# Performance work log

Hardware: AMD Instinct MI355X
Metric: run time of the kernel (lower is better)

The kernel has to match this reference:

```python
import jax, jax.numpy as jnp
import numpy as np

B, T, H, N_HEADS, HEAD_D = 16, 512, 1024, 16, 64
N_SKILLS, N_ITEMS = 50, 1000
VOCAB = 4 + 2 * N_ITEMS  # 2004
LN_EPS = 1e-3            # keras LayerNormalization default
PAD_NEG = -float(2 ** 32)


def position_encoding(length, hidden):
    # official transformer get_position_encoding: [sin | cos], then interleaved
    half = hidden // 2
    pos = jnp.arange(length, dtype=jnp.float32)[:, None]
    log_inc = np.log(1e4) / (half - 1)
    inv_ts = jnp.exp(jnp.arange(half, dtype=jnp.float32) * -log_inc)
    ang = pos * inv_ts[None, :]  # [T, H/2]
    pe = jnp.zeros((length, hidden), dtype=jnp.float32)
    pe = pe.at[:, 0::2].set(jnp.sin(ang))
    pe = pe.at[:, 1::2].set(jnp.cos(ang))
    return pe


def setup_inputs() -> dict:
    key = jax.random.key(0)
    ks = jax.random.split(key, 12)
    rng = np.random.default_rng(0)
    # binary Q-matrix [skills, items]; ensure every item has >=1 skill
    Qb = (rng.random((N_SKILLS, N_ITEMS)) < 0.1).astype(np.float32)
    Qb[rng.integers(0, N_SKILLS, size=N_ITEMS), np.arange(N_ITEMS)] = 1.0
    s = 0.02
    return {
        'prob_x': jax.random.randint(ks[0], (B, T), 4, VOCAB, dtype=jnp.int32),
        'prob_y2': jax.random.randint(ks[1], (B, T), 4, VOCAB, dtype=jnp.int32),
        'emb': jax.random.normal(ks[2], (VOCAB, H), jnp.float32) * s,
        'wq': jax.random.normal(ks[3], (H, N_HEADS, HEAD_D), jnp.float32) * s,
        'wk': jax.random.normal(ks[4], (H, N_HEADS, HEAD_D), jnp.float32) * s,
        'wv': jax.random.normal(ks[5], (H, N_HEADS, HEAD_D), jnp.float32) * s,
        'wo': jax.random.normal(ks[6], (N_HEADS, HEAD_D, H), jnp.float32) * s,
        'ln_gamma': jnp.ones((H,), jnp.float32),
        'ln_beta': jnp.zeros((H,), jnp.float32),
        'w_hid': jax.random.normal(ks[7], (H, 2 * N_SKILLS), jnp.float32) * s,
        'b_hid': jnp.zeros((2 * N_SKILLS,), jnp.float32),
        'w_skill': jax.random.normal(ks[8], (2 * N_SKILLS, N_SKILLS), jnp.float32) * s,
        'b_skill': jnp.zeros((N_SKILLS,), jnp.float32),
        'w_prob': jax.random.normal(ks[9], (N_SKILLS, N_ITEMS), jnp.float32) * s,
        'b_prob': jnp.zeros((N_ITEMS,), jnp.float32),
        'q_matrix': jnp.asarray(Qb),
    }


def reference(prob_x, prob_y2, emb, wq, wk, wv, wo, ln_gamma, ln_beta,
              w_hid, b_hid, w_skill, b_skill, w_prob, b_prob, q_matrix):
    Bq, Tq = prob_x.shape
    pid = (prob_x - 4) // 2        # item ids [B,T]
    next_pid = (prob_y2 - 4) // 2  # [B,T]

    x = emb[prob_x] + position_encoding(Tq, emb.shape[1])  # [B,T,H]

    # QKV projections (DenseEinsum, no bias)
    q = jnp.einsum('bth,hnd->btnd', x, wq) * (HEAD_D ** -0.5)
    k = jnp.einsum('bth,hnd->btnd', x, wk)
    v = jnp.einsum('bth,hnd->btnd', x, wv)

    logits = jnp.einsum('btnd,bfnd->bnft', k, q)  # [B,N,F,T]

    # causal future mask: 0 on/below diag, -inf above (1 - exp(1/tri - 1))
    causal = jnp.where(jnp.tril(jnp.ones((Tq, Tq), bool)), 0.0, -jnp.inf)
    logits = logits + causal[None, None]

    # item-item common-skill mask: -inf where items share no skill, 0 otherwise
    qtq = q_matrix.T @ q_matrix  # [I,I]
    items_items = jnp.where(qtq > 0, 0.0, -jnp.inf)
    sub = items_items[pid[:, 1:, None], pid[:, None, 1:]]  # [B,T-1,T-1]
    csm = jnp.pad(sub, ((0, 0), (1, 0), (1, 0)), constant_values=PAD_NEG)
    logits = logits + csm[:, None]  # broadcast over heads

    weights = jax.nn.softmax(logits, axis=-1)  # [B,N,F,T]
    attn = jnp.einsum('bnft,btnd->bfnd', weights, v)
    attn = jnp.einsum('bfnd,ndh->bfh', attn, wo)

    # add & layer-norm (keras default eps=1e-3)
    y = x + attn
    mu = jnp.mean(y, axis=-1, keepdims=True)
    var = jnp.var(y, axis=-1, keepdims=True)
    y = (y - mu) * jax.lax.rsqrt(var + LN_EPS) * ln_gamma + ln_beta

    h = jax.nn.relu(y @ w_hid + b_hid)
    skills = h @ w_skill + b_skill
    problems = jax.nn.sigmoid(skills @ w_prob + b_prob)  # [B,T,I]
    # einsum('abi,abi->ab', problems, one_hot(next_pid)) == gather
    out = jnp.take_along_axis(problems, next_pid[..., None], axis=-1)[..., 0]
    return out
```

## Files before the change

kernel.cpp:

```cpp
#include <hip/hip_runtime.h>
#include <hip/hip_bf16.h>

#define Bb 16
#define Tt 512
#define Hh 1024
#define NHd 16
#define HD 64
#define BT (Bb*Tt)
#define NSK 50
#define NIT 1000

typedef __attribute__((ext_vector_type(8))) short bf16x8;
typedef __attribute__((ext_vector_type(4))) float f32x4;
typedef unsigned short u16;
typedef unsigned int u32;
typedef unsigned long long u64;

__device__ inline u16 f2bf(float x){
  union { float f; u32 u; } v; v.f = x;
  u32 r = v.u + 0x7fffu + ((v.u >> 16) & 1u);
  return (u16)(r >> 16);
}
__device__ inline float bf2f(u32 u){
  union { u32 uu; float f; } v; v.uu = u << 16; return v.f;
}
__device__ inline u32 pack2bf(float lo, float hi){
  return (u32)f2bf(lo) | ((u32)f2bf(hi) << 16);
}
__device__ inline void gload_lds16(const void* g, void* l){
  __builtin_amdgcn_global_load_lds(
    (const __attribute__((address_space(1))) u32*)g,
    (__attribute__((address_space(3))) u32*)l, 16, 0, 0);
}

__global__ __launch_bounds__(256) void k_wT_all(
    const float* __restrict__ wq, const float* __restrict__ wk,
    const float* __restrict__ wv, const float* __restrict__ wo,
    const float* __restrict__ wh, const float* __restrict__ gamma,
    const float* __restrict__ beta,
    const int* __restrict__ prob_x, const float* __restrict__ qm,
    const float* __restrict__ wp,
    u16* __restrict__ wqkvT, u16* __restrict__ woT, u16* __restrict__ whT,
    float2* __restrict__ uvp, u64* __restrict__ pmask, float* __restrict__ wpt){
  int z = blockIdx.z;
  int tid = threadIdx.x;
  if (z == 5){
    if (blockIdx.y) return;
    int i = blockIdx.x*256 + tid;
    int pid = (prob_x[i] - 4) >> 1;
    u64 m = 0ull;
    #pragma unroll
    for (int s = 0; s < NSK; s++)
      if (qm[s*NIT + pid] != 0.f) m |= (1ull << s);
    pmask[i] = m;
    return;
  }
  if (z == 6){
    int blk = blockIdx.y*32 + blockIdx.x;
    if (blk >= 250) return;
    int p = blk*4 + (tid >> 6), lane = tid & 63;
    if (lane < NSK) wpt[(size_t)p*64 + lane] = wp[(size_t)lane*NIT + p];
    return;
  }
  const float* src; u16* dst; int C = 1024; float scale = 1.f; bool useg = false;
  if      (z == 0){ src = wq; dst = wqkvT;                       scale = 0.125f; }
  else if (z == 1){ src = wk; dst = wqkvT + (size_t)1024*1024; }
  else if (z == 2){ src = wv; dst = wqkvT + (size_t)2*1024*1024; }
  else if (z == 3){ src = wo; dst = woT; }
  else            { src = wh; dst = whT; C = 100; useg = true; if (blockIdx.x >= 4) return; }

  __shared__ float tile[32][33];
  int tx = tid & 31, ty = tid >> 5;
  int c0 = blockIdx.x*32, r0 = blockIdx.y*32;
  #pragma unroll
  for (int i = 0; i < 32; i += 8){
    int r = r0 + ty + i, cc = c0 + tx;
    tile[ty+i][tx] = (cc < C) ? src[(size_t)r*C + cc] : 0.f;
  }
  __syncthreads();
  float gmul = useg ? gamma[r0 + tx] : scale;
  #pragma unroll
  for (int i = 0; i < 32; i += 8){
    int cc = c0 + ty + i, rr = r0 + tx;
    dst[(size_t)cc*1024 + rr] = f2bf(tile[tx][ty+i] * gmul);
  }
  if (useg && tid < 32){
    int j = tid;
    float us = 0.f, vs = 0.f;
    #pragma unroll
    for (int k = 0; k < 32; k++){
      float wv2 = tile[k][j];
      us += gamma[r0 + k] * wv2;
      vs += beta[r0 + k] * wv2;
    }
    uvp[(size_t)blockIdx.y*128 + c0 + j] = make_float2(us, vs);
  }
}

__global__ __launch_bounds__(256) void k_build_x2(
    const int* __restrict__ prob_x, const float* __restrict__ emb,
    u16* __restrict__ xb){
  int bt = blockIdx.x, tid = threadIdx.x;
  int t = bt & (Tt-1);
  int ix = prob_x[bt];
  int h = tid*4;
  float4 e = *(const float4*)(emb + (size_t)ix*Hh + h);
  const float LOG_INC = 0.0180241495f;
  int j0 = h >> 1;
  float a0 = (float)t * __expf(-(float)j0 * LOG_INC);
  float a1 = (float)t * __expf(-(float)(j0+1) * LOG_INC);
  alignas(8) u16 tmp[4] = { f2bf(e.x + __sinf(a0)), f2bf(e.y + __cosf(a0)),
                            f2bf(e.z + __sinf(a1)), f2bf(e.w + __cosf(a1)) };
  *(uint2*)(xb + (size_t)bt*Hh + h) = *(const uint2*)tmp;
}

#define MFMA_(d, va, vb) d = __builtin_amdgcn_mfma_f32_16x16x32_bf16(va, vb, d, 0, 0, 0)

__device__ __forceinline__ void gemm128x256_core(
    const u16* __restrict__ A, const u16* __restrict__ Bt,
    int row0, int col0, char* lds, f32x4 (&acc)[4][4])
{
  const int tid = threadIdx.x, w = tid >> 6, lane = tid & 63;
  const int c = lane & 15, g = lane >> 4;
  const int wm = w >> 2, wn = w & 3;
  const int srl = lane >> 3, scb = lane & 7;
  const int kbsw = scb ^ srl;

  #define STAGE6(buf, k0)                                                        \
    do {                                                                         \
      char* _da = lds + (buf)*49152 + w*2048;                                    \
      char* _db = lds + (buf)*49152 + 16384 + w*4096;                            \
      _Pragma("unroll")                                                          \
      for (int i = 0; i < 2; i++)                                                \
        gload_lds16(A + (size_t)(row0 + 16*w + 8*i + srl)*1024 + (k0) + kbsw*8,  \
                    _da + i*1024);                                               \
      _Pragma("unroll")                                                          \
      for (int i = 0; i < 4; i++)                                                \
        gload_lds16(Bt + (size_t)(col0 + 32*w + 8*i + srl)*1024 + (k0) + kbsw*8, \
                    _db + i*1024);                                               \
    } while (0)

  STAGE6(0, 0);
  STAGE6(1, 64);
  asm volatile("s_waitcnt vmcnt(6)" ::: "memory");
  __builtin_amdgcn_s_barrier();

  #pragma unroll
  for (int kt = 0; kt < 16; ++kt){
    const int buf = kt % 3;
    if (kt + 2 < 16) STAGE6((kt + 2) % 3, (kt + 2)*64);

    bf16x8 af[2][4], bf[2][4];
    #pragma unroll
    for (int kh = 0; kh < 2; kh++){
      #pragma unroll
      for (int mi = 0; mi < 4; mi++){
        int r = 64*wm + 16*mi + c;
        af[kh][mi] = *(const bf16x8*)(lds + buf*49152 + r*128 + (((kh*4 + g) ^ (c & 7))*16));
      }
      #pragma unroll
      for (int ni = 0; ni < 4; ni++){
        int r = 64*wn + 16*ni + c;
        bf[kh][ni] = *(const bf16x8*)(lds + buf*49152 + 16384 + r*128 + (((kh*4 + g) ^ (c & 7))*16));
      }
    }
    __builtin_amdgcn_s_setprio(1);
    #pragma unroll
    for (int kh = 0; kh < 2; kh++)
      #pragma unroll
      for (int mi = 0; mi < 4; mi++)
        #pragma unroll
        for (int ni = 0; ni < 4; ni++) MFMA_(acc[mi][ni], af[kh][mi], bf[kh][ni]);
    __builtin_amdgcn_s_setprio(0);

    if (kt < 15){
      if (kt < 14) asm volatile("s_waitcnt vmcnt(6)" ::: "memory");
      else         asm volatile("s_waitcnt vmcnt(0)" ::: "memory");
      __builtin_amdgcn_s_barrier();
    }
  }
  #undef STAGE6
}

__global__ __launch_bounds__(512) void k_gemm_qkv3(
    const u16* __restrict__ A, const u16* __restrict__ Bt,
    u16* __restrict__ qb, u16* __restrict__ kb, u16* __restrict__ vtb)
{
  extern __shared__ char lds[];
  int lin = blockIdx.x;
  int xcd = lin & 7, j = lin >> 3;
  int by = xcd*8 + (j & 7);
  int bx = j >> 3;
  const int row0 = by*128, col0 = bx*256;

  f32x4 acc[4][4];
  #pragma unroll
  for (int mi = 0; mi < 4; mi++)
    #pragma unroll
    for (int ni = 0; ni < 4; ni++) acc[mi][ni] = (f32x4){0.f,0.f,0.f,0.f};

  gemm128x256_core(A, Bt, row0, col0, lds, acc);

  const int tid = threadIdx.x, w = tid >> 6, lane = tid & 63;
  const int c = lane & 15, g = lane >> 4;
  const int wm = w >> 2, wn = w & 3;
  int seg = col0 >> 10;
  int colL0 = col0 & 1023;
  if (seg < 2){
    u16* C = seg ? kb : qb;
    #pragma unroll
    for (int mi = 0; mi < 4; mi++){
      int m0 = row0 + 64*wm + 16*mi + 4*g;
      int bb = m0 >> 9, t0 = m0 & (Tt-1);
      #pragma unroll
      for (int ni = 0; ni < 4; ni++){
        int col = colL0 + 64*wn + 16*ni + c;
        int hd_ = col >> 6, d_ = col & 63;
        u16* base = C + (((size_t)bb*NHd + hd_)*Tt + t0)*HD + d_;
        #pragma unroll
        for (int r = 0; r < 4; r++) base[(size_t)r*HD] = f2bf(acc[mi][ni][r]);
      }
    }
  } else {
    #pragma unroll
    for (int mi = 0; mi < 4; mi++){
      int m0 = row0 + 64*wm + 16*mi + 4*g;
      int bb = m0 >> 9, t0 = m0 & (Tt-1);
      #pragma unroll
      for (int ni = 0; ni < 4; ni++){
        int col = colL0 + 64*wn + 16*ni + c;
        int hd_ = col >> 6, d_ = col & 63;
        alignas(8) u16 tmp[4];
        #pragma unroll
        for (int r = 0; r < 4; r++) tmp[r] = f2bf(acc[mi][ni][r]);
        *(uint2*)(vtb + (((size_t)bb*NHd + hd_)*HD + d_)*Tt + t0) = *(const uint2*)tmp;
      }
    }
  }
}

__global__ __launch_bounds__(512) void k_gemm_wo3(
    const u16* __restrict__ A, const u16* __restrict__ Bt,
    u16* __restrict__ C, const u16* __restrict__ res, float2* __restrict__ stats)
{
  extern __shared__ char lds[];
  int lin = blockIdx.x;
  int xcd = lin & 7, j = lin >> 3;
  int by = xcd*8 + (j & 7);
  int bx = j >> 3;
  const int row0 = by*128, col0 = bx*256;

  f32x4 acc[4][4];
  #pragma unroll
  for (int mi = 0; mi < 4; mi++)
    #pragma unroll
    for (int ni = 0; ni < 4; ni++) acc[mi][ni] = (f32x4){0.f,0.f,0.f,0.f};

  gemm128x256_core(A, Bt, row0, col0, lds, acc);

  const int tid = threadIdx.x, w = tid >> 6, lane = tid & 63;
  const int c = lane & 15, g = lane >> 4;
  const int wm = w >> 2, wn = w & 3;

  float s1[4][4], s2[4][4];
  #pragma unroll
  for (int mi = 0; mi < 4; mi++)
    #pragma unroll
    for (int r = 0; r < 4; r++){ s1[mi][r] = 0.f; s2[mi][r] = 0.f; }

  #pragma unroll
  for (int mi = 0; mi < 4; mi++){
    int m0 = row0 + 64*wm + 16*mi + 4*g;
    #pragma unroll
    for (int ni = 0; ni < 4; ni++){
      int col = col0 + 64*wn + 16*ni + c;
      #pragma unroll
      for (int r = 0; r < 4; r++){
        size_t idx = (size_t)(m0 + r)*Hh + col;
        float yv = acc[mi][ni][r] + bf2f((u32)res[idx]);
        C[idx] = f2bf(yv);
        s1[mi][r] += yv; s2[mi][r] += yv*yv;
      }
    }
  }
  #pragma unroll
  for (int mi = 0; mi < 4; mi++)
    #pragma unroll
    for (int r = 0; r < 4; r++){
      #pragma unroll
      for (int off = 1; off < 16; off <<= 1){
        s1[mi][r] += __shfl_xor(s1[mi][r], off);
        s2[mi][r] += __shfl_xor(s2[mi][r], off);
      }
    }
  __syncthreads();
  float (*sStat)[4][2] = (float(*)[4][2])lds;
  if (c == 0){
    #pragma unroll
    for (int mi = 0; mi < 4; mi++)
      #pragma unroll
      for (int r = 0; r < 4; r++){
        int ml = 64*wm + 16*mi + 4*g + r;
        sStat[ml][wn][0] = s1[mi][r];
        sStat[ml][wn][1] = s2[mi][r];
      }
  }
  __syncthreads();
  if (tid < 128){
    float a = sStat[tid][0][0] + sStat[tid][1][0] + sStat[tid][2][0] + sStat[tid][3][0];
    float b = sStat[tid][0][1] + sStat[tid][1][1] + sStat[tid][2][1] + sStat[tid][3][1];
    stats[(size_t)(row0 + tid)*4 + bx] = make_float2(a, b);
  }
}

__global__ __launch_bounds__(256) void k_gemm_hidden(
    const u16* __restrict__ A, const u16* __restrict__ Bt,
    const float2* __restrict__ stats, const float2* __restrict__ uvp,
    const float* __restrict__ b_hid, u16* __restrict__ C)
{
  __shared__ u16 sA[32*64];
  __shared__ u16 sB[128*64];
  __shared__ float sMu[32][2];
  __shared__ float2 sUV[128];
  const int tid = threadIdx.x, w = tid >> 6, lane = tid & 63;
  const int c = lane & 15, g = lane >> 4;
  const int row0 = blockIdx.x*32;
  const int srl = lane >> 3, scb = lane & 7;

  if (tid < 32){
    float m = 0.f, q = 0.f;
    #pragma unroll
    for (int cb = 0; cb < 4; cb++){
      float2 s = stats[(size_t)(row0 + tid)*4 + cb];
      m += s.x; q += s.y;
    }
    float mu = m * (1.f/Hh);
    float var = q * (1.f/Hh) - mu*mu;
    sMu[tid][0] = mu;
    sMu[tid][1] = rsqrtf(var + 1e-3f);
  }
  if (tid < 128){
    float us = 0.f, vs = 0.f;
    #pragma unroll 8
    for (int cb = 0; cb < 32; cb++){
      float2 p = uvp[(size_t)cb*128 + tid];
      us += p.x; vs += p.y;
    }
    float2 r = make_float2(0.f, 0.f);
    if (tid < 100){ r.x = us; r.y = vs + b_hid[tid]; }
    sUV[tid] = r;
  }

  f32x4 acc[2][2];
  #pragma unroll
  for (int mi = 0; mi < 2; mi++)
    #pragma unroll
    for (int ni = 0; ni < 2; ni++) acc[mi][ni] = (f32x4){0.f,0.f,0.f,0.f};

  for (int k0 = 0; k0 < 1024; k0 += 64){
    __syncthreads();
    {
      int arow = 8*w + srl;
      int kblk = scb ^ (arow & 7);
      gload_lds16(A + (size_t)(row0 + arow)*1024 + k0 + kblk*8,
                  (char*)sA + w*1024);
      #pragma unroll
      for (int i = 0; i < 4; i++){
        int brow = 32*w + 8*i + srl;
        int kb2 = scb ^ (brow & 7);
        gload_lds16(Bt + (size_t)brow*1024 + k0 + kb2*8,
                    (char*)sB + w*4096 + i*1024);
      }
    }
    __syncthreads();

    #pragma unroll
    for (int kh = 0; kh < 2; kh++){
      bf16x8 af[2], bf[2];
      #pragma unroll
      for (int mi = 0; mi < 2; mi++){
        int r = 16*mi + c;
        af[mi] = *(const bf16x8*)((char*)sA + r*128 + (((4*kh + g) ^ (r & 7))*16));
      }
      #pragma unroll
      for (int ni = 0; ni < 2; ni++){
        int r = 32*w + 16*ni + c;
        bf[ni] = *(const bf16x8*)((char*)sB + r*128 + (((4*kh + g) ^ (r & 7))*16));
      }
      #pragma unroll
      for (int mi = 0; mi < 2; mi++)
        #pragma unroll
        for (int ni = 0; ni < 2; ni++)
          acc[mi][ni] = __builtin_amdgcn_mfma_f32_16x16x32_bf16(af[mi], bf[ni], acc[mi][ni], 0, 0, 0);
    }
  }

  #pragma unroll
  for (int mi = 0; mi < 2; mi++){
    #pragma unroll
    for (int ni = 0; ni < 2; ni++){
      int col = 32*w + 16*ni + c;
      float2 uvv = sUV[col];
      #pragma unroll
      for (int r = 0; r < 4; r++){
        int ml = 16*mi + 4*g + r;
        float mu = sMu[ml][0], inv = sMu[ml][1];
        float h = fmaxf(inv*(acc[mi][ni][r] - mu*uvv.x) + uvv.y, 0.f);
        C[(size_t)(row0 + ml)*128 + col] = f2bf(h);
      }
    }
  }
}

__global__ __launch_bounds__(256, 3) void k_flash(
    const u16* __restrict__ qb, const u16* __restrict__ kb,
    const u16* __restrict__ vtb, const u64* __restrict__ pmask,
    u16* __restrict__ o)
{
  __shared__ u16 sK[2][64*64];
  __shared__ u16 sV[2][64*64];
  __shared__ u16 sP[4][32*64];

  const int tid = threadIdx.x;
  const int w = tid >> 6, lane = tid & 63;
  const int c = lane & 15, g = lane >> 4;
  const int bn = blockIdx.x;
  const int Fblk = 3 - blockIdx.y;
  const int b = bn >> 4, n = bn & 15;
  const int f0w = Fblk*128 + w*32;

  bf16x8 qf[2][2];
  #pragma unroll
  for (int fb = 0; fb < 2; fb++){
    const u16* qrow = qb + ((size_t)bn*Tt + f0w + 16*fb + c)*HD + 8*g;
    qf[fb][0] = *(const bf16x8*)(qrow);
    qf[fb][1] = *(const bf16x8*)(qrow + 32);
  }

  const u64* pmb = pmask + b*Tt;
  int frow[2]; u64 mf[2];
  #pragma unroll
  for (int fb = 0; fb < 2; fb++){ frow[fb] = f0w + 16*fb + c; mf[fb] = pmb[frow[fb]]; }

  f32x4 O[2][4];
  #pragma unroll
  for (int fb = 0; fb < 2; fb++)
    #pragma unroll
    for (int dt = 0; dt < 4; dt++) O[fb][dt] = (f32x4){0.f,0.f,0.f,0.f};
  float m_run[2] = {-1e30f, -1e30f};
  float l_run[2] = {0.f, 0.f};

  const char* kbase = (const char*)(kb + (size_t)bn*Tt*HD);
  const char* vbase = (const char*)(vtb + (size_t)bn*HD*Tt);
  char* sPw = (char*)(sP[w]);

  const int srow0 = 16*w + (lane >> 3);
  const int scb = lane & 7;

  #define STAGE(buf, T0)                                                          \
    {                                                                             \
      _Pragma("unroll")                                                           \
      for (int i = 0; i < 2; i++){                                                \
        int row = srow0 + 8*i;                                                    \
        int cb = scb ^ (row & 7);                                                 \
        gload_lds16(kbase + (size_t)((T0) + row)*128 + cb*16,                     \
                    (char*)sK[buf] + w*2048 + i*1024);                            \
        gload_lds16(vbase + (size_t)row*1024 + (T0)*2 + cb*16,                    \
                    (char*)sV[buf] + w*2048 + i*1024);                            \
      }                                                                           \
    }

  const int nT = 2*Fblk + 2;
  STAGE(0, 0)
  __syncthreads();
  int cur = 0;

  for (int it = 0; it < nT; ++it){
    const int t0 = it * 64;
    if (it + 1 < nT) STAGE(cur^1, (it+1)*64)

    if (t0 <= f0w + 31){
      const char* sKc = (const char*)sK[cur];
      const char* sVc = (const char*)sV[cur];

      f32x4 S[2][4];
      __builtin_amdgcn_s_setprio(1);
      #pragma unroll
      for (int ts = 0; ts < 4; ts++){
        int tl = ts*16 + c;
        const char* kr = sKc + tl*128;
        int sw = (tl & 7) << 4;
        bf16x8 kf0 = *(const bf16x8*)(kr + ((g*16) ^ sw));
        bf16x8 kf1 = *(const bf16x8*)(kr + ((64 + g*16) ^ sw));
        #pragma unroll
        for (int fb = 0; fb < 2; fb++){
          f32x4 a = (f32x4){0.f,0.f,0.f,0.f};
          a = __builtin_amdgcn_mfma_f32_16x16x32_bf16(kf0, qf[fb][0], a, 0, 0, 0);
          a = __builtin_amdgcn_mfma_f32_16x16x32_bf16(kf1, qf[fb][1], a, 0, 0, 0);
          S[fb][ts] = a;
        }
      }
      __builtin_amdgcn_s_setprio(0);

      u64 pmt[4][4];
      #pragma unroll
      for (int ts = 0; ts < 4; ts++){
        const u64* pp = pmb + t0 + 16*ts + 4*g;
        pmt[ts][0] = pp[0]; pmt[ts][1] = pp[1];
        pmt[ts][2] = pp[2]; pmt[ts][3] = pp[3];
      }

      #pragma unroll
      for (int fb = 0; fb < 2; fb++){
        int f = frow[fb];
        u64 mfr = mf[fb];
        #pragma unroll
        for (int ts = 0; ts < 4; ts++){
          #pragma unroll
          for (int r = 0; r < 4; r++){
            int t = t0 + 16*ts + 4*g + r;
            bool ok = (f == 0) ? (t == 0)
                     : (t > 0 && t <= f && ((pmt[ts][r] & mfr) != 0ull));
            if (!ok) S[fb][ts][r] = -1e30f;
          }
        }
        float mx = -1e30f;
        #pragma unroll
        for (int ts = 0; ts < 4; ts++)
          #pragma unroll
          for (int r = 0; r < 4; r++) mx = fmaxf(mx, S[fb][ts][r]);
        mx = fmaxf(mx, __shfl_xor(mx, 16));
        mx = fmaxf(mx, __shfl_xor(mx, 32));
        float mnew = fmaxf(m_run[fb], mx);
        float al = __expf(m_run[fb] - mnew);
        m_run[fb] = mnew;
        l_run[fb] *= al;
        #pragma unroll
        for (int dt = 0; dt < 4; dt++) O[fb][dt] *= al;

        int prow = 16*fb + c;
        int swz = (prow & 7) << 4;
        float lsum = 0.f;
        #pragma unroll
        for (int ts = 0; ts < 4; ts++){
          float p0 = __expf(S[fb][ts][0] - mnew);
          float p1 = __expf(S[fb][ts][1] - mnew);
          float p2 = __expf(S[fb][ts][2] - mnew);
          float p3 = __expf(S[fb][ts][3] - mnew);
          lsum += (p0 + p1) + (p2 + p3);
          uint2 dw = { pack2bf(p0, p1), pack2bf(p2, p3) };
          *(uint2*)(sPw + prow*128 + ((32*ts + 8*g) ^ swz)) = dw;
        }
        l_run[fb] += lsum;
      }

      bf16x8 pa[2][2];
      #pragma unroll
      for (int fb = 0; fb < 2; fb++){
        int prow = 16*fb + c;
        int swz = (prow & 7) << 4;
        const char* pr = sPw + prow*128;
        pa[fb][0] = *(const bf16x8*)(pr + ((16*g) ^ swz));
        pa[fb][1] = *(const bf16x8*)(pr + ((64 + 16*g) ^ swz));
      }
      __builtin_amdgcn_s_setprio(1);
      #pragma unroll
      for (int dt = 0; dt < 4; dt++){
        int vl = dt*16 + c;
        const char* vr = sVc + vl*128;
        int swv = (vl & 7) << 4;
        bf16x8 vf0 = *(const bf16x8*)(vr + ((g*16) ^ swv));
        bf16x8 vf1 = *(const bf16x8*)(vr + ((64 + g*16) ^ swv));
        #pragma unroll
        for (int fb = 0; fb < 2; fb++){
          O[fb][dt] = __builtin_amdgcn_mfma_f32_16x16x32_bf16(vf0, pa[fb][0], O[fb][dt], 0, 0, 0);
          O[fb][dt] = __builtin_amdgcn_mfma_f32_16x16x32_bf16(vf1, pa[fb][1], O[fb][dt], 0, 0, 0);
        }
      }
      __builtin_amdgcn_s_setprio(0);
    }

    __syncthreads();
    cur ^= 1;
  }
  #undef STAGE

  #pragma unroll
  for (int fb = 0; fb < 2; fb++){
    float l = l_run[fb];
    l += __shfl_xor(l, 16);
    l += __shfl_xor(l, 32);
    float inv = 1.f / l;
    u16* ob = o + ((size_t)(b*Tt + frow[fb]))*Hh + n*HD;
    #pragma unroll
    for (int dt = 0; dt < 4; dt++){
      alignas(8) u16 tmp[4];
      #pragma unroll
      for (int r = 0; r < 4; r++) tmp[r] = f2bf(O[fb][dt][r] * inv);
      *(uint2*)(ob + dt*16 + 4*g) = *(const uint2*)tmp;
    }
  }
}

__global__ __launch_bounds__(256) void k_tail(
    const u16* __restrict__ hidden, const int* __restrict__ prob_y2,
    const float* __restrict__ w_skill, const float* __restrict__ b_skill,
    const float* __restrict__ wpt, const float* __restrict__ b_prob,
    float* __restrict__ out)
{
  __shared__ float shid[4][104];
  int w = threadIdx.x >> 6, lane = threadIdx.x & 63;
  int row = blockIdx.x*4 + w;
  if (lane < 50){
    u32 hp = *(const u32*)(hidden + (size_t)row*128 + 2*lane);
    shid[w][2*lane]   = bf2f(hp & 0xffffu);
    shid[w][2*lane+1] = bf2f(hp >> 16);
  }
  __syncthreads();
  float s = 0.f;
  if (lane < 50){
    s = b_skill[lane];
    #pragma unroll 4
    for (int i = 0; i < 100; i++) s += shid[w][i] * w_skill[i*NSK + lane];
  }
  int np = (prob_y2[row] - 4) >> 1;
  float z = (lane < 50) ? s * wpt[(size_t)np*64 + lane] : 0.f;
  #pragma unroll
  for (int off = 1; off < 64; off <<= 1) z += __shfl_xor(z, off);
  if (lane == 0) out[row] = 1.f/(1.f + expf(-(z + b_prob[np])));
}

extern "C" void kernel_launch(void* const* d_in, const int* in_sizes, int n_in,
                              void* d_out, int out_size, void* d_ws, size_t ws_size,
                              hipStream_t stream)
{
  const int*   prob_x   = (const int*)d_in[0];
  const int*   prob_y2  = (const int*)d_in[1];
  const float* emb      = (const float*)d_in[2];
  const float* wq       = (const float*)d_in[3];
  const float* wk       = (const float*)d_in[4];
  const float* wv       = (const float*)d_in[5];
  const float* wo       = (const float*)d_in[6];
  const float* ln_g     = (const float*)d_in[7];
  const float* ln_b     = (const float*)d_in[8];
  const float* w_hid    = (const float*)d_in[9];
  const float* b_hid    = (const float*)d_in[10];
  const float* w_skill  = (const float*)d_in[11];
  const float* b_skill  = (const float*)d_in[12];
  const float* w_prob   = (const float*)d_in[13];
  const float* b_prob   = (const float*)d_in[14];
  const float* q_matrix = (const float*)d_in[15];
  float* out = (float*)d_out;

  char* ws = (char*)d_ws;
  const size_t M16 = (size_t)BT*Hh*2;
  u16*   xb     = (u16*)(ws);
  u16*   qb     = (u16*)(ws + M16);
  u16*   kb     = (u16*)(ws + 2*M16);
  u16*   vtb    = (u16*)(ws + 3*M16);
  u16*   att    = (u16*)(ws + 4*M16);
  u16*   y      = qb;
  u16*   hidden = kb;
  char*  aux    = ws + 5*M16;
  u16*   wqkvT  = (u16*)(aux);
  u16*   woT    = wqkvT + (size_t)3*1024*1024;
  u16*   whT    = woT + (size_t)1024*1024;
  float* wpt    = (float*)(whT + (size_t)128*1024);
  u64*   pmask  = (u64*)(wpt + (size_t)NIT*64);
  float2* stats = (float2*)((char*)pmask + (size_t)BT*8);
  float2* uvp   = (float2*)((char*)stats + (size_t)BT*8*sizeof(float2));

  k_wT_all<<<dim3(32,32,7), 256, 0, stream>>>(wq, wk, wv, wo, w_hid, ln_g, ln_b,
                                              prob_x, q_matrix, w_prob,
                                              wqkvT, woT, whT, uvp, pmask, wpt);
  k_build_x2<<<BT, 256, 0, stream>>>(prob_x, emb, xb);

  k_gemm_qkv3<<<768, 512, 147456, stream>>>(xb, wqkvT, qb, kb, vtb);

  k_flash<<<dim3(Bb*NHd, 4), 256, 0, stream>>>(qb, kb, vtb, pmask, att);

  k_gemm_wo3<<<256, 512, 147456, stream>>>(att, woT, y, xb, stats);

  k_gemm_hidden<<<256, 256, 0, stream>>>(y, whT, stats, uvp, b_hid, hidden);

  k_tail<<<BT/4, 256, 0, stream>>>(hidden, prob_y2, w_skill, b_skill, wpt, b_prob, out);
}
```

Before: 168.8 us.

## Fuse embedding build and tail into other kernels; cheapen flash masking and rescale

Folds the embedding+position-encoding build into the weight-prep launch and fuses the skill/problem tail into the hidden GEMM epilogue, keeping hidden activations in LDS instead of global memory. Removes two kernel launches and a global round trip. In the flash kernel, fully-causal tiles take a simpler mask path, and the online-softmax rescale is skipped unless the max grows by more than a threshold, reducing exp and multiply work. Lazy rescaling allows larger unnormalized exponentials, which costs some numeric headroom.

```diff
diff --git a/kernel.cpp b/kernel.cpp
--- a/kernel.cpp
+++ b/kernel.cpp
@@ -39,9 +39,10 @@
     const float* __restrict__ wh, const float* __restrict__ gamma,
     const float* __restrict__ beta,
     const int* __restrict__ prob_x, const float* __restrict__ qm,
-    const float* __restrict__ wp,
+    const float* __restrict__ wp, const float* __restrict__ emb,
     u16* __restrict__ wqkvT, u16* __restrict__ woT, u16* __restrict__ whT,
-    float2* __restrict__ uvp, u64* __restrict__ pmask, float* __restrict__ wpt){
+    float2* __restrict__ uvp, u64* __restrict__ pmask, float* __restrict__ wpt,
+    u16* __restrict__ xb){
   int z = blockIdx.z;
   int tid = threadIdx.x;
   if (z == 5){
@@ -62,6 +63,25 @@
     if (lane < NSK) wpt[(size_t)p*64 + lane] = wp[(size_t)lane*NIT + p];
     return;
   }
+  if (z == 7){
+    int blk = blockIdx.y*32 + blockIdx.x;
+    int h = tid*4, j0 = h >> 1;
+    const float LOG_INC = 0.0180241495f;
+    float e0 = __expf(-(float)j0 * LOG_INC);
+    float e1 = __expf(-(float)(j0+1) * LOG_INC);
+    #pragma unroll
+    for (int rr = 0; rr < 8; rr++){
+      int bt = blk*8 + rr;
+      int t = bt & (Tt-1);
+      int ix = prob_x[bt];
+      float4 e = *(const float4*)(emb + (size_t)ix*Hh + h);
+      float a0 = (float)t * e0, a1 = (float)t * e1;
+      alignas(8) u16 tmp[4] = { f2bf(e.x + __sinf(a0)), f2bf(e.y + __cosf(a0)),
+                                f2bf(e.z + __sinf(a1)), f2bf(e.w + __cosf(a1)) };
+      *(uint2*)(xb + (size_t)bt*Hh + h) = *(const uint2*)tmp;
+    }
+    return;
+  }
   const float* src; u16* dst; int C = 1024; float scale = 1.f; bool useg = false;
   if      (z == 0){ src = wq; dst = wqkvT;                       scale = 0.125f; }
   else if (z == 1){ src = wk; dst = wqkvT + (size_t)1024*1024; }
@@ -95,23 +115,6 @@
     }
     uvp[(size_t)blockIdx.y*128 + c0 + j] = make_float2(us, vs);
   }
-}
-
-__global__ __launch_bounds__(256) void k_build_x2(
-    const int* __restrict__ prob_x, const float* __restrict__ emb,
-    u16* __restrict__ xb){
-  int bt = blockIdx.x, tid = threadIdx.x;
-  int t = bt & (Tt-1);
-  int ix = prob_x[bt];
-  int h = tid*4;
-  float4 e = *(const float4*)(emb + (size_t)ix*Hh + h);
-  const float LOG_INC = 0.0180241495f;
-  int j0 = h >> 1;
-  float a0 = (float)t * __expf(-(float)j0 * LOG_INC);
-  float a1 = (float)t * __expf(-(float)(j0+1) * LOG_INC);
-  alignas(8) u16 tmp[4] = { f2bf(e.x + __sinf(a0)), f2bf(e.y + __cosf(a0)),
-                            f2bf(e.z + __sinf(a1)), f2bf(e.w + __cosf(a1)) };
-  *(uint2*)(xb + (size_t)bt*Hh + h) = *(const uint2*)tmp;
 }
 
 #define MFMA_(d, va, vb) d = __builtin_amdgcn_mfma_f32_16x16x32_bf16(va, vb, d, 0, 0, 0)
@@ -316,7 +319,10 @@
 __global__ __launch_bounds__(256) void k_gemm_hidden(
     const u16* __restrict__ A, const u16* __restrict__ Bt,
     const float2* __restrict__ stats, const float2* __restrict__ uvp,
-    const float* __restrict__ b_hid, u16* __restrict__ C)
+    const float* __restrict__ b_hid, const int* __restrict__ prob_y2,
+    const float* __restrict__ w_skill, const float* __restrict__ b_skill,
+    const float* __restrict__ wpt, const float* __restrict__ b_prob,
+    float* __restrict__ out)
 {
   __shared__ u16 sA[32*64];
   __shared__ u16 sB[128*64];
@@ -395,6 +401,8 @@
     }
   }
 
+  __syncthreads();
+  float* sHf = (float*)sB;
   #pragma unroll
   for (int mi = 0; mi < 2; mi++){
     #pragma unroll
@@ -405,10 +413,28 @@
       for (int r = 0; r < 4; r++){
         int ml = 16*mi + 4*g + r;
         float mu = sMu[ml][0], inv = sMu[ml][1];
-        float h = fmaxf(inv*(acc[mi][ni][r] - mu*uvv.x) + uvv.y, 0.f);
-        C[(size_t)(row0 + ml)*128 + col] = f2bf(h);
-      }
-    }
+        sHf[ml*128 + col] = fmaxf(inv*(acc[mi][ni][r] - mu*uvv.x) + uvv.y, 0.f);
+      }
+    }
+  }
+  __syncthreads();
+
+  {
+    int row = tid >> 3, sub = tid & 7;
+    int bt = row0 + row;
+    int np = (prob_y2[bt] - 4) >> 1;
+    const float* hrow = sHf + row*128;
+    float z = 0.f;
+    for (int jj = sub; jj < NSK; jj += 8){
+      float s = b_skill[jj];
+      #pragma unroll 4
+      for (int i = 0; i < 100; i++) s += hrow[i] * w_skill[i*NSK + jj];
+      z += s * wpt[(size_t)np*64 + jj];
+    }
+    z += __shfl_xor(z, 1);
+    z += __shfl_xor(z, 2);
+    z += __shfl_xor(z, 4);
+    if (sub == 0) out[bt] = 1.f/(1.f + __expf(-(z + b_prob[np])));
   }
 }
 
@@ -482,6 +508,7 @@
     if (t0 <= f0w + 31){
       const char* sKc = (const char*)sK[cur];
       const char* sVc = (const char*)sV[cur];
+      const bool fullcausal = (t0 >= 64) && (t0 + 63 <= f0w);
 
       f32x4 S[2][4];
       __builtin_amdgcn_s_setprio(1);
@@ -514,14 +541,22 @@
       for (int fb = 0; fb < 2; fb++){
         int f = frow[fb];
         u64 mfr = mf[fb];
-        #pragma unroll
-        for (int ts = 0; ts < 4; ts++){
+        if (fullcausal){
           #pragma unroll
-          for (int r = 0; r < 4; r++){
-            int t = t0 + 16*ts + 4*g + r;
-            bool ok = (f == 0) ? (t == 0)
-                     : (t > 0 && t <= f && ((pmt[ts][r] & mfr) != 0ull));
-            if (!ok) S[fb][ts][r] = -1e30f;
+          for (int ts = 0; ts < 4; ts++)
+            #pragma unroll
+            for (int r = 0; r < 4; r++)
+              if (!(pmt[ts][r] & mfr)) S[fb][ts][r] = -1e30f;
+        } else {
+          #pragma unroll
+          for (int ts = 0; ts < 4; ts++){
+            #pragma unroll
+            for (int r = 0; r < 4; r++){
+              int t = t0 + 16*ts + 4*g + r;
+              bool ok = (f == 0) ? (t == 0)
+                       : (t > 0 && t <= f && ((pmt[ts][r] & mfr) != 0ull));
+              if (!ok) S[fb][ts][r] = -1e30f;
+            }
           }
         }
         float mx = -1e30f;
@@ -531,12 +566,18 @@
           for (int r = 0; r < 4; r++) mx = fmaxf(mx, S[fb][ts][r]);
         mx = fmaxf(mx, __shfl_xor(mx, 16));
         mx = fmaxf(mx, __shfl_xor(mx, 32));
-        float mnew = fmaxf(m_run[fb], mx);
-        float al = __expf(m_run[fb] - mnew);
-        m_run[fb] = mnew;
-        l_run[fb] *= al;
-        #pragma unroll
-        for (int dt = 0; dt < 4; dt++) O[fb][dt] *= al;
+
+        float mnew;
+        if (__all(mx <= m_run[fb] + 8.f)){
+          mnew = m_run[fb];
+        } else {
+          mnew = fmaxf(m_run[fb], mx);
+          float al = __expf(m_run[fb] - mnew);
+          m_run[fb] = mnew;
+          l_run[fb] *= al;
+          #pragma unroll
+          for (int dt = 0; dt < 4; dt++) O[fb][dt] *= al;
+        }
 
         int prow = 16*fb + c;
         int swz = (prow & 7) << 4;
@@ -600,34 +641,6 @@
       *(uint2*)(ob + dt*16 + 4*g) = *(const uint2*)tmp;
     }
   }
-}
-
-__global__ __launch_bounds__(256) void k_tail(
-    const u16* __restrict__ hidden, const int* __restrict__ prob_y2,
-    const float* __restrict__ w_skill, const float* __restrict__ b_skill,
-    const float* __restrict__ wpt, const float* __restrict__ b_prob,
-    float* __restrict__ out)
-{
-  __shared__ float shid[4][104];
-  int w = threadIdx.x >> 6, lane = threadIdx.x & 63;
-  int row = blockIdx.x*4 + w;
-  if (lane < 50){
-    u32 hp = *(const u32*)(hidden + (size_t)row*128 + 2*lane);
-    shid[w][2*lane]   = bf2f(hp & 0xffffu);
-    shid[w][2*lane+1] = bf2f(hp >> 16);
-  }
-  __syncthreads();
-  float s = 0.f;
-  if (lane < 50){
-    s = b_skill[lane];
-    #pragma unroll 4
-    for (int i = 0; i < 100; i++) s += shid[w][i] * w_skill[i*NSK + lane];
-  }
-  int np = (prob_y2[row] - 4) >> 1;
-  float z = (lane < 50) ? s * wpt[(size_t)np*64 + lane] : 0.f;
-  #pragma unroll
-  for (int off = 1; off < 64; off <<= 1) z += __shfl_xor(z, off);
-  if (lane == 0) out[row] = 1.f/(1.f + expf(-(z + b_prob[np])));
 }
 
 extern "C" void kernel_launch(void* const* d_in, const int* in_sizes, int n_in,
@@ -660,7 +673,6 @@
   u16*   vtb    = (u16*)(ws + 3*M16);
   u16*   att    = (u16*)(ws + 4*M16);
   u16*   y      = qb;
-  u16*   hidden = kb;
   char*  aux    = ws + 5*M16;
   u16*   wqkvT  = (u16*)(aux);
   u16*   woT    = wqkvT + (size_t)3*1024*1024;
@@ -670,10 +682,9 @@
   float2* stats = (float2*)((char*)pmask + (size_t)BT*8);
   float2* uvp   = (float2*)((char*)stats + (size_t)BT*8*sizeof(float2));
 
-  k_wT_all<<<dim3(32,32,7), 256, 0, stream>>>(wq, wk, wv, wo, w_hid, ln_g, ln_b,
-                                              prob_x, q_matrix, w_prob,
-                                              wqkvT, woT, whT, uvp, pmask, wpt);
-  k_build_x2<<<BT, 256, 0, stream>>>(prob_x, emb, xb);
+  k_wT_all<<<dim3(32,32,8), 256, 0, stream>>>(wq, wk, wv, wo, w_hid, ln_g, ln_b,
+                                              prob_x, q_matrix, w_prob, emb,
+                                              wqkvT, woT, whT, uvp, pmask, wpt, xb);
 
   k_gemm_qkv3<<<768, 512, 147456, stream>>>(xb, wqkvT, qb, kb, vtb);
 
@@ -681,7 +692,6 @@
 
   k_gemm_wo3<<<256, 512, 147456, stream>>>(att, woT, y, xb, stats);
 
-  k_gemm_hidden<<<256, 256, 0, stream>>>(y, whT, stats, uvp, b_hid, hidden);
-
-  k_tail<<<BT/4, 256, 0, stream>>>(hidden, prob_y2, w_skill, b_skill, wpt, b_prob, out);
-}
+  k_gemm_hidden<<<256, 256, 0, stream>>>(y, whT, stats, uvp, b_hid,
+                                         prob_y2, w_skill, b_skill, wpt, b_prob, out);
+}
```

After: 185.6 us. 9.9% more time.
